# Kernel tuning notes

Measured on AMD Instinct MI355X. Metric: run time of the kernel, lower is better.

The kernel has to match this reference:

```python
import jax, jax.numpy as jnp
import numpy as np

N_NODES = 100000
N_EDGES = 3200000
P = 32
Q = 32
D = P + Q


def setup_inputs() -> dict:
    key = jax.random.key(0)
    ks = jax.random.split(key, 10)
    u = jax.random.normal(ks[0], (N_NODES, D), dtype=jnp.float32)
    intensity = jax.random.normal(ks[1], (N_NODES, Q), dtype=jnp.float32)
    edge_src = jax.random.randint(ks[2], (N_EDGES,), 0, N_NODES, dtype=jnp.int32)
    edge_dst = jax.random.randint(ks[3], (N_EDGES,), 0, N_NODES, dtype=jnp.int32)
    std = 0.1  # matches nn.init.normal_(std=0.1)
    Wf = std * jax.random.normal(ks[4], (D, D), dtype=jnp.float32)
    Wg = std * jax.random.normal(ks[5], (D, D), dtype=jnp.float32)
    Wz = std * jax.random.normal(ks[6], (P, D), dtype=jnp.float32)
    WA = std * jax.random.normal(ks[7], (Q, 2 * Q), dtype=jnp.float32)
    return {
        "u": u, "intensity": intensity,
        "edge_src": edge_src, "edge_dst": edge_dst,
        "Wf": Wf, "bf": jnp.zeros((D,), jnp.float32),
        "Wg": Wg, "bg": jnp.zeros((D,), jnp.float32),
        "Wz": Wz, "bz": jnp.zeros((P,), jnp.float32),
        "WA": WA, "bA": jnp.zeros((Q,), jnp.float32),
    }


def reference(u, intensity, edge_src, edge_dst, Wf, bf, Wg, bg, Wz, bz, WA, bA):
    N = u.shape[0]
    p = Wz.shape[0]
    # neighbor mean of intensity (zeros for isolated nodes)
    nbr_sum = jax.ops.segment_sum(intensity[edge_src], edge_dst, num_segments=N)
    deg = jax.ops.segment_sum(jnp.ones(edge_src.shape, intensity.dtype), edge_dst, num_segments=N)
    nbr_mean = jnp.where(deg[:, None] > 0, nbr_sum / jnp.maximum(deg, 1.0)[:, None], 0.0)
    # aggout = ReLU(A([intensity_i ; mean_nbr_i]))
    aggout = jax.nn.relu(jnp.concatenate([intensity, nbr_mean], axis=1) @ WA.T + bA)
    Fu = jax.nn.softplus(u @ Wf.T + bf)
    Gu = jax.nn.softplus(u @ Wg.T + bg)
    Zu = jnp.tanh(u @ Wz.T + bz)
    du = -Fu * u + Gu * jnp.concatenate([Zu, aggout], axis=1)
    up = u[:, :p]
    dup = du[:, :p]
    duq = du[:, p:]
    # project dup to be orthogonal to up (norm-preserving drift)
    dup = dup - (jnp.sum(dup * up, axis=1, keepdims=True) / jnp.sum(up * up, axis=1, keepdims=True)) * up
    return jnp.concatenate([dup, duq], axis=1)
```

## Files before the change

### kernel.cpp

```cpp
#include <hip/hip_runtime.h>


#define RLOG 7
#define RNODES 128
#define NBLK 512
#define CAP 6144
#define CHUNK 6272
#define CVB 64

typedef __attribute__((ext_vector_type(8))) short short8;
typedef __attribute__((ext_vector_type(4))) float f32x4;
typedef __attribute__((ext_vector_type(2))) float f32x2;

__device__ __forceinline__ unsigned short f2bf(float x) {
    union { float f; unsigned u; } v; v.f = x;
    unsigned r = v.u + 0x7FFF + ((v.u >> 16) & 1);
    return (unsigned short)(r >> 16);
}

#if __has_builtin(__builtin_amdgcn_cvt_pk_fp8_f32) && __has_builtin(__builtin_amdgcn_cvt_pk_f32_fp8)
__device__ __forceinline__ unsigned pack4_fp8(float a, float b, float c, float d) {
    int p = __builtin_amdgcn_cvt_pk_fp8_f32(a, b, 0, false);
    p = __builtin_amdgcn_cvt_pk_fp8_f32(c, d, p, true);
    return (unsigned)p;
}
__device__ __forceinline__ void unpack4_fp8(unsigned w, float& a, float& b, float& c, float& d) {
    f32x2 lo = __builtin_amdgcn_cvt_pk_f32_fp8(w, false);
    f32x2 hi = __builtin_amdgcn_cvt_pk_f32_fp8(w, true);
    a = lo[0]; b = lo[1]; c = hi[0]; d = hi[1];
}
#else
__device__ __forceinline__ unsigned char f2fp8_sw(float x) {
    union { float f; unsigned u; } v; v.f = x;
    unsigned s = (v.u >> 24) & 0x80;
    float ax = fminf(fabsf(x), 448.0f);
    union { float f; unsigned u; } w; w.f = ax;
    int e = (int)((w.u >> 23) & 0xFF) - 127;
    if (e < -6) {
        int mi = (int)(ax * 512.0f + 0.5f);
        if (mi > 7) mi = 7;
        return (unsigned char)(s | mi);
    }
    unsigned mant = (w.u >> 20) & 7;
    unsigned rest = w.u & 0xFFFFF;
    unsigned rnd = (rest > 0x80000u) || (rest == 0x80000u && (mant & 1));
    unsigned enc = ((unsigned)(e + 7) << 3) | mant;
    enc += rnd;
    if (enc > 0x7Eu) enc = 0x7Eu;
    return (unsigned char)(s | enc);
}
__device__ __forceinline__ float fp82f_sw(unsigned char b) {
    unsigned e = (b >> 3) & 0xF, m = b & 7;
    float mag;
    if (e == 0) mag = (float)m * 0.001953125f;
    else {
        union { unsigned u; float f; } v;
        v.u = ((e + 120u) << 23) | (m << 20);
        mag = v.f;
    }
    return (b & 0x80) ? -mag : mag;
}
__device__ __forceinline__ unsigned pack4_fp8(float a, float b, float c, float d) {
    return (unsigned)f2fp8_sw(a) | ((unsigned)f2fp8_sw(b) << 8) |
           ((unsigned)f2fp8_sw(c) << 16) | ((unsigned)f2fp8_sw(d) << 24);
}
__device__ __forceinline__ void unpack4_fp8(unsigned w, float& a, float& b, float& c, float& d) {
    a = fp82f_sw((unsigned char)(w & 0xFF));
    b = fp82f_sw((unsigned char)((w >> 8) & 0xFF));
    c = fp82f_sw((unsigned char)((w >> 16) & 0xFF));
    d = fp82f_sw((unsigned char)((w >> 24) & 0xFF));
}
#endif

__device__ __forceinline__ float softplus_fast(float x) {
    float t = __expf(-fabsf(x));
    return fmaxf(x, 0.0f) + __logf(1.0f + t);
}

__device__ __forceinline__ float tanh_fast(float x) {
    float t = __expf(-2.0f * fabsf(x));
    float m = (1.0f - t) * __builtin_amdgcn_rcpf(1.0f + t);
    return __builtin_copysignf(m, x);
}

__device__ __forceinline__ int chunk_of(int E) {
    return (((E + NBLK - 1) / NBLK) + 3) & ~3;
}

__global__ __launch_bounds__(1024) void prep_count(
    const int* __restrict__ edst, int* __restrict__ cnt,
    const float* __restrict__ x, unsigned short* __restrict__ ybf,
    unsigned* __restrict__ yfp8, int total4,
    const float* __restrict__ Wf, const float* __restrict__ Wg,
    const float* __restrict__ Wz, const float* __restrict__ WA,
    unsigned short* __restrict__ wbig,
    int E, int B) {
    int tid = threadIdx.x, blk = blockIdx.x;
    if (blk < NBLK) {
        __shared__ int lcnt[1024];
        for (int b = tid; b < B; b += 1024) lcnt[b] = 0;
        __syncthreads();
        int chunk = chunk_of(E);
        int start = blk * chunk;
        int end = min(E, start + chunk);
        int v4s = start >> 2, v4e = end >> 2;
        for (int i = v4s + tid; i < v4e; i += 1024) {
            int4 d = ((const int4*)edst)[i];
            atomicAdd(&lcnt[d.x >> RLOG], 1);
            atomicAdd(&lcnt[d.y >> RLOG], 1);
            atomicAdd(&lcnt[d.z >> RLOG], 1);
            atomicAdd(&lcnt[d.w >> RLOG], 1);
        }
        for (int i = (v4e << 2) + tid; i < end; i += 1024)
            atomicAdd(&lcnt[edst[i] >> RLOG], 1);
        __syncthreads();
        for (int b = tid; b < B; b += 1024) cnt[b * NBLK + blk] = lcnt[b];
    } else if (blk < NBLK + CVB) {
        int cb = blk - NBLK;
        for (int i = cb * 1024 + tid; i < total4; i += CVB * 1024) {
            float4 v = ((const float4*)x)[i];
            ushort4 r;
            r.x = f2bf(v.x); r.y = f2bf(v.y); r.z = f2bf(v.z); r.w = f2bf(v.w);
            ((ushort4*)ybf)[i] = r;
            yfp8[i] = pack4_fp8(v.x, v.y, v.z, v.w);
        }
    } else {
        for (int idx = tid; idx < 192 * 64; idx += 1024) {
            int r = idx >> 6, k = idx & 63;
            float v = (r < 64)  ? Wf[r * 64 + k]
                    : (r < 128) ? Wg[(r - 64) * 64 + k]
                    : (r < 160) ? Wz[(r - 128) * 64 + k]
                                : WA[(r - 160) * 64 + k];
            wbig[idx] = f2bf(v);
        }
    }
}

__global__ __launch_bounds__(512) void scanA(const int* __restrict__ cnt,
                                             int* __restrict__ lofs,
                                             int* __restrict__ T) {
    int t = threadIdx.x, b = blockIdx.x;
    int lane = t & 63, wave = t >> 6;
    int v = cnt[b * NBLK + t];
    int incl = v;
    #pragma unroll
    for (int off = 1; off < 64; off <<= 1) {
        int w = __shfl_up(incl, off);
        if (lane >= off) incl += w;
    }
    __shared__ int wt[8];
    if (lane == 63) wt[wave] = incl;
    __syncthreads();
    int woff = 0;
    for (int i = 0; i < wave; ++i) woff += wt[i];
    int excl = woff + incl - v;
    lofs[b * NBLK + t] = excl;
    if (t == NBLK - 1) T[b] = excl + v;
}

__global__ __launch_bounds__(1024) void scanB(const int* __restrict__ T,
                                              int* __restrict__ G, int B) {
    int t = threadIdx.x;
    int lane = t & 63, wave = t >> 6;
    int v = (t < B) ? T[t] : 0;
    int incl = v;
    #pragma unroll
    for (int off = 1; off < 64; off <<= 1) {
        int w = __shfl_up(incl, off);
        if (lane >= off) incl += w;
    }
    __shared__ int wt[16];
    if (lane == 63) wt[wave] = incl;
    __syncthreads();
    int woff = 0;
    for (int i = 0; i < wave; ++i) woff += wt[i];
    if (t < B) G[t] = woff + incl - v;
}

__global__ __launch_bounds__(1024) void bin_scatter(const int* __restrict__ esrc,
                                                    const int* __restrict__ edst,
                                                    const int* __restrict__ cnt,
                                                    const int* __restrict__ lofs,
                                                    const int* __restrict__ G,
                                                    int* __restrict__ binned,
                                                    int E, int B) {
    __shared__ unsigned sl_pack[CHUNK];
    __shared__ unsigned short sl_bkt[CHUNK];
    __shared__ int lsc[1024];
    __shared__ int base[1024];
    __shared__ int wtot[16];
    int tid = threadIdx.x, blk = blockIdx.x;
    int lane = tid & 63, wave = tid >> 6;

    int v = (tid < B) ? cnt[tid * NBLK + blk] : 0;
    int incl = v;
    #pragma unroll
    for (int off = 1; off < 64; off <<= 1) {
        int w = __shfl_up(incl, off);
        if (lane >= off) incl += w;
    }
    if (lane == 63) wtot[wave] = incl;
    __syncthreads();
    int woff = 0;
    for (int i = 0; i < wave; ++i) woff += wtot[i];
    int excl = woff + incl - v;
    if (tid < B) {
        base[tid] = G[tid] + lofs[tid * NBLK + blk] - excl;
        lsc[tid] = excl;
    }
    __syncthreads();

    int chunk = chunk_of(E);
    int start = blk * chunk;
    int end = min(E, start + chunk);
    int m = end - start;
    int v4s = start >> 2, v4e = end >> 2;
    for (int i = v4s + tid; i < v4e; i += 1024) {
        int4 d = ((const int4*)edst)[i];
        int4 s = ((const int4*)esrc)[i];
        int b0 = d.x >> RLOG, b1 = d.y >> RLOG, b2 = d.z >> RLOG, b3 = d.w >> RLOG;
        int p0 = atomicAdd(&lsc[b0], 1);
        int p1 = atomicAdd(&lsc[b1], 1);
        int p2 = atomicAdd(&lsc[b2], 1);
        int p3 = atomicAdd(&lsc[b3], 1);
        sl_pack[p0] = ((unsigned)(d.x & (RNODES - 1)) << 17) | (unsigned)s.x;
        sl_pack[p1] = ((unsigned)(d.y & (RNODES - 1)) << 17) | (unsigned)s.y;
        sl_pack[p2] = ((unsigned)(d.z & (RNODES - 1)) << 17) | (unsigned)s.z;
        sl_pack[p3] = ((unsigned)(d.w & (RNODES - 1)) << 17) | (unsigned)s.w;
        sl_bkt[p0] = (unsigned short)b0;
        sl_bkt[p1] = (unsigned short)b1;
        sl_bkt[p2] = (unsigned short)b2;
        sl_bkt[p3] = (unsigned short)b3;
    }
    for (int i = (v4e << 2) + tid; i < end; i += 1024) {
        int d = edst[i];
        int s = esrc[i];
        int b = d >> RLOG;
        int p = atomicAdd(&lsc[b], 1);
        sl_pack[p] = ((unsigned)(d & (RNODES - 1)) << 17) | (unsigned)s;
        sl_bkt[p] = (unsigned short)b;
    }
    __syncthreads();

    for (int i = tid; i < m; i += 1024) {
        binned[base[sl_bkt[i]] + i] = (int)sl_pack[i];
    }
}

__global__ __launch_bounds__(1024) void bucket_fused(
    const int* __restrict__ binned, const int* __restrict__ G,
    const unsigned* __restrict__ ifp8,
    unsigned short* __restrict__ xnbr, int E, int N, int B) {
    __shared__ int sl[CAP];
    __shared__ int sl2[CAP];
    __shared__ int c128[RNODES];
    __shared__ int pos[RNODES];
    __shared__ int dstart[RNODES];
    __shared__ int ddeg[RNODES];
    int tid = threadIdx.x;
    int b = blockIdx.x;
    int start = G[b];
    int end = (b + 1 < B) ? G[b + 1] : E;
    int m = min(end - start, CAP);

    for (int i = tid; i < m; i += 1024) sl[i] = binned[start + i];
    if (tid < RNODES) c128[tid] = 0;
    __syncthreads();
    for (int i = tid; i < m; i += 1024) atomicAdd(&c128[sl[i] >> 17], 1);
    __syncthreads();

    int x = 0, incl = 0;
    if (tid < RNODES) { x = c128[tid]; incl = x; }
    #pragma unroll
    for (int off = 1; off < RNODES; off <<= 1) {
        int y = 0;
        if (tid < RNODES && tid >= off) y = c128[tid - off];
        __syncthreads();
        if (tid < RNODES) { incl += y; c128[tid] = incl; }
        __syncthreads();
    }
    if (tid < RNODES) {
        int excl = incl - x;
        pos[tid] = excl;
        dstart[tid] = excl;
        ddeg[tid] = x;
    }
    __syncthreads();
    for (int i = tid; i < m; i += 1024) {
        int e = sl[i];
        int p = atomicAdd(&pos[e >> 17], 1);
        sl2[p] = e & 131071;
    }
    __syncthreads();

    int g = tid >> 3;
    int fl = tid & 7;
    int node = b * RNODES + g;
    int st = dstart[g];
    int dg = ddeg[g];
    float a0 = 0.f, a1 = 0.f, a2 = 0.f, a3 = 0.f;
    int j = 0;
    for (; j + 3 < dg; j += 4) {
        int s0 = sl2[st + j];
        int s1 = sl2[st + j + 1];
        int s2 = sl2[st + j + 2];
        int s3 = sl2[st + j + 3];
        unsigned w0 = ifp8[(size_t)s0 * 8 + fl];
        unsigned w1 = ifp8[(size_t)s1 * 8 + fl];
        unsigned w2 = ifp8[(size_t)s2 * 8 + fl];
        unsigned w3 = ifp8[(size_t)s3 * 8 + fl];
        float x0, x1, x2, x3;
        unpack4_fp8(w0, x0, x1, x2, x3);
        a0 += x0; a1 += x1; a2 += x2; a3 += x3;
        unpack4_fp8(w1, x0, x1, x2, x3);
        a0 += x0; a1 += x1; a2 += x2; a3 += x3;
        unpack4_fp8(w2, x0, x1, x2, x3);
        a0 += x0; a1 += x1; a2 += x2; a3 += x3;
        unpack4_fp8(w3, x0, x1, x2, x3);
        a0 += x0; a1 += x1; a2 += x2; a3 += x3;
    }
    for (; j < dg; ++j) {
        int s0 = sl2[st + j];
        unsigned w0 = ifp8[(size_t)s0 * 8 + fl];
        float x0, x1, x2, x3;
        unpack4_fp8(w0, x0, x1, x2, x3);
        a0 += x0; a1 += x1; a2 += x2; a3 += x3;
    }
    if (node < N) {
        float inv = (dg > 0) ? 1.0f / (float)dg : 0.0f;
        ushort4 r;
        r.x = f2bf(a0 * inv); r.y = f2bf(a1 * inv);
        r.z = f2bf(a2 * inv); r.w = f2bf(a3 * inv);
        ((ushort4*)xnbr)[(size_t)node * 8 + fl] = r;
    }
}

__global__ __launch_bounds__(256, 4) void node_mfma(
    const float* __restrict__ u,
    const unsigned short* __restrict__ ibf,
    const unsigned short* __restrict__ xnbr,
    const unsigned short* __restrict__ wbig,
    const float* __restrict__ bfp, const float* __restrict__ bgp,
    const float* __restrict__ bzp, const float* __restrict__ bAp,
    float* __restrict__ out, int N) {
    int tid = threadIdx.x;
    int lane = tid & 63;
    int wave = tid >> 6;
    int tile = blockIdx.x * 4 + wave;
    int ntiles = N >> 4;
    if (tile >= ntiles) return;

    int col = lane & 15;
    int kg = lane >> 4;
    int n0 = tile * 16;
    int node = n0 + col;

    const float* ub = u + (size_t)node * 64 + kg * 8;
    float4 u0 = *(const float4*)(ub);
    float4 u1 = *(const float4*)(ub + 4);
    float4 u2 = *(const float4*)(ub + 32);
    float4 u3 = *(const float4*)(ub + 36);
    short8 au0, au1;
    au0[0]=(short)f2bf(u0.x); au0[1]=(short)f2bf(u0.y); au0[2]=(short)f2bf(u0.z); au0[3]=(short)f2bf(u0.w);
    au0[4]=(short)f2bf(u1.x); au0[5]=(short)f2bf(u1.y); au0[6]=(short)f2bf(u1.z); au0[7]=(short)f2bf(u1.w);
    au1[0]=(short)f2bf(u2.x); au1[1]=(short)f2bf(u2.y); au1[2]=(short)f2bf(u2.z); au1[3]=(short)f2bf(u2.w);
    au1[4]=(short)f2bf(u3.x); au1[5]=(short)f2bf(u3.y); au1[6]=(short)f2bf(u3.z); au1[7]=(short)f2bf(u3.w);
    short8 ax0 = *(const short8*)(ibf  + (size_t)node * 32 + kg * 8);
    short8 ax1 = *(const short8*)(xnbr + (size_t)node * 32 + kg * 8);

    const short8* wb = (const short8*)wbig;
    f32x4 acc[12];
    #pragma unroll
    for (int t = 0; t < 12; ++t) acc[t] = (f32x4){0.f, 0.f, 0.f, 0.f};
    #pragma unroll
    for (int t = 0; t < 12; ++t) {
        short8 a0 = (t < 10) ? au0 : ax0;
        short8 a1 = (t < 10) ? au1 : ax1;
        short8 b0 = wb[(t * 16 + col) * 8 + kg];
        short8 b1 = wb[(t * 16 + col) * 8 + 4 + kg];
        acc[t] = __builtin_amdgcn_mfma_f32_16x16x32_bf16(a0, b0, acc[t], 0, 0, 0);
        acc[t] = __builtin_amdgcn_mfma_f32_16x16x32_bf16(a1, b1, acc[t], 0, 0, 0);
    }

    float bfv[4], bgv[4], bzv[4];
    #pragma unroll
    for (int s = 0; s < 4; ++s) {
        int j = s * 16 + col;
        bfv[s] = bfp[j];
        bgv[s] = bgp[j];
        bzv[s] = (s < 2) ? bzp[j] : bAp[j - 32];
    }

    float du01[2][4], uv01[2][4];
    float ar[4], br[4];
    #pragma unroll
    for (int r = 0; r < 4; ++r) { ar[r] = 0.f; br[r] = 0.f; }
    #pragma unroll
    for (int s = 0; s < 2; ++s) {
        #pragma unroll
        for (int r = 0; r < 4; ++r) {
            int nd = n0 + kg * 4 + r;
            float uu = u[(size_t)nd * 64 + s * 16 + col];
            float fpre = acc[s][r] + bfv[s];
            float gpre = acc[4 + s][r] + bgv[s];
            float zpre = acc[8 + s][r] + bzv[s];
            float Fu = softplus_fast(fpre);
            float Gu = softplus_fast(gpre);
            float zv = tanh_fast(zpre);
            float d = -Fu * uu + Gu * zv;
            du01[s][r] = d;
            uv01[s][r] = uu;
            ar[r] = fmaf(d, uu, ar[r]);
            br[r] = fmaf(uu, uu, br[r]);
        }
    }
    #pragma unroll
    for (int off = 1; off < 16; off <<= 1) {
        #pragma unroll
        for (int r = 0; r < 4; ++r) {
            ar[r] += __shfl_xor(ar[r], off);
            br[r] += __shfl_xor(br[r], off);
        }
    }
    float coef[4];
    #pragma unroll
    for (int r = 0; r < 4; ++r) coef[r] = ar[r] * __builtin_amdgcn_rcpf(br[r]);

    #pragma unroll
    for (int s = 0; s < 2; ++s) {
        #pragma unroll
        for (int r = 0; r < 4; ++r) {
            int nd = n0 + kg * 4 + r;
            out[(size_t)nd * 64 + s * 16 + col] = du01[s][r] - coef[r] * uv01[s][r];
        }
    }
    #pragma unroll
    for (int s = 2; s < 4; ++s) {
        #pragma unroll
        for (int r = 0; r < 4; ++r) {
            int nd = n0 + kg * 4 + r;
            float uu = u[(size_t)nd * 64 + s * 16 + col];
            float fpre = acc[s][r] + bfv[s];
            float gpre = acc[4 + s][r] + bgv[s];
            float zpre = acc[8 + s][r] + bzv[s];
            float Fu = softplus_fast(fpre);
            float Gu = softplus_fast(gpre);
            float zv = fmaxf(zpre, 0.0f);
            out[(size_t)nd * 64 + s * 16 + col] = -Fu * uu + Gu * zv;
        }
    }
}

extern "C" void kernel_launch(void* const* d_in, const int* in_sizes, int n_in,
                              void* d_out, int out_size, void* d_ws, size_t ws_size,
                              hipStream_t stream) {
    const float* u         = (const float*)d_in[0];
    const float* intensity = (const float*)d_in[1];
    const int*   esrc      = (const int*)d_in[2];
    const int*   edst      = (const int*)d_in[3];
    const float* Wf        = (const float*)d_in[4];
    const float* bf        = (const float*)d_in[5];
    const float* Wg        = (const float*)d_in[6];
    const float* bg        = (const float*)d_in[7];
    const float* Wz        = (const float*)d_in[8];
    const float* bz        = (const float*)d_in[9];
    const float* WA        = (const float*)d_in[10];
    const float* bA        = (const float*)d_in[11];

    int N = in_sizes[0] / 64;
    int E = in_sizes[2];
    int B = (N + RNODES - 1) / RNODES;
    int M = B * NBLK;

    int* cnt    = (int*)d_ws;
    int* lofs   = cnt + M;
    int* T      = lofs + M;
    int* G      = T + 1024;
    int* binned = G + 1024;
    unsigned short* xnbr = (unsigned short*)(binned + E);
    unsigned short* wbig = xnbr + (size_t)N * 32;
    unsigned short* ibf  = wbig + 192 * 64;
    unsigned* ifp8 = (unsigned*)(ibf + (size_t)N * 32);

    prep_count<<<NBLK + CVB + 1, 1024, 0, stream>>>(
        edst, cnt, intensity, ibf, ifp8, N * 8, Wf, Wg, Wz, WA, wbig, E, B);
    scanA<<<B, 512, 0, stream>>>(cnt, lofs, T);
    scanB<<<1, 1024, 0, stream>>>(T, G, B);
    bin_scatter<<<NBLK, 1024, 0, stream>>>(esrc, edst, cnt, lofs, G, binned, E, B);
    bucket_fused<<<B, 1024, 0, stream>>>(binned, G, ifp8, xnbr, E, N, B);
    int ntiles = N / 16;
    int nblocks = (ntiles + 3) / 4;
    node_mfma<<<nblocks, 256, 0, stream>>>(u, ibf, xnbr, wbig,
                                           bf, bg, bz, bA, (float*)d_out, N);
}
```

Baseline: 98.04 us.

## Fold scanB into consumers and widen the neighbor gather to 8-byte loads

Drops the single-block scanB launch. bin_scatter and bucket_fused each now rescan the per-bucket totals T in shared memory to get global bucket offsets, which removes one kernel launch and its serialization point at the cost of redundant scan work in every block. The bucket_fused gather is also restructured: each 8-lane group splits into two halves that process alternate edges with uint2 loads of 8 fp8 values, then combine through a shuffle-xor. The aim is more bytes per load and more memory-level parallelism per node, paid for with extra accumulator registers and a reduction step.

```diff
diff --git a/kernel.cpp b/kernel.cpp
--- a/kernel.cpp
+++ b/kernel.cpp
@@ -158,30 +158,11 @@
     if (t == NBLK - 1) T[b] = excl + v;
 }
 
-__global__ __launch_bounds__(1024) void scanB(const int* __restrict__ T,
-                                              int* __restrict__ G, int B) {
-    int t = threadIdx.x;
-    int lane = t & 63, wave = t >> 6;
-    int v = (t < B) ? T[t] : 0;
-    int incl = v;
-    #pragma unroll
-    for (int off = 1; off < 64; off <<= 1) {
-        int w = __shfl_up(incl, off);
-        if (lane >= off) incl += w;
-    }
-    __shared__ int wt[16];
-    if (lane == 63) wt[wave] = incl;
-    __syncthreads();
-    int woff = 0;
-    for (int i = 0; i < wave; ++i) woff += wt[i];
-    if (t < B) G[t] = woff + incl - v;
-}
-
 __global__ __launch_bounds__(1024) void bin_scatter(const int* __restrict__ esrc,
                                                     const int* __restrict__ edst,
                                                     const int* __restrict__ cnt,
                                                     const int* __restrict__ lofs,
-                                                    const int* __restrict__ G,
+                                                    const int* __restrict__ T,
                                                     int* __restrict__ binned,
                                                     int E, int B) {
     __shared__ unsigned sl_pack[CHUNK];
@@ -192,6 +173,20 @@
     int tid = threadIdx.x, blk = blockIdx.x;
     int lane = tid & 63, wave = tid >> 6;
 
+    int tv = (tid < B) ? T[tid] : 0;
+    int tincl = tv;
+    #pragma unroll
+    for (int off = 1; off < 64; off <<= 1) {
+        int w = __shfl_up(tincl, off);
+        if (lane >= off) tincl += w;
+    }
+    if (lane == 63) wtot[wave] = tincl;
+    __syncthreads();
+    int twoff = 0;
+    for (int i = 0; i < wave; ++i) twoff += wtot[i];
+    int Gv = twoff + tincl - tv;
+    __syncthreads();
+
     int v = (tid < B) ? cnt[tid * NBLK + blk] : 0;
     int incl = v;
     #pragma unroll
@@ -205,7 +200,7 @@
     for (int i = 0; i < wave; ++i) woff += wtot[i];
     int excl = woff + incl - v;
     if (tid < B) {
-        base[tid] = G[tid] + lofs[tid * NBLK + blk] - excl;
+        base[tid] = Gv + lofs[tid * NBLK + blk] - excl;
         lsc[tid] = excl;
     }
     __syncthreads();
@@ -248,7 +243,7 @@
 }
 
 __global__ __launch_bounds__(1024) void bucket_fused(
-    const int* __restrict__ binned, const int* __restrict__ G,
+    const int* __restrict__ binned, const int* __restrict__ T,
     const unsigned* __restrict__ ifp8,
     unsigned short* __restrict__ xnbr, int E, int N, int B) {
     __shared__ int sl[CAP];
@@ -257,11 +252,27 @@
     __shared__ int pos[RNODES];
     __shared__ int dstart[RNODES];
     __shared__ int ddeg[RNODES];
+    __shared__ int wtot[16];
+    __shared__ int s_start;
     int tid = threadIdx.x;
     int b = blockIdx.x;
-    int start = G[b];
-    int end = (b + 1 < B) ? G[b + 1] : E;
-    int m = min(end - start, CAP);
+    int lane = tid & 63, wave = tid >> 6;
+
+    int tv = (tid < B) ? T[tid] : 0;
+    int tincl = tv;
+    #pragma unroll
+    for (int off = 1; off < 64; off <<= 1) {
+        int w = __shfl_up(tincl, off);
+        if (lane >= off) tincl += w;
+    }
+    if (lane == 63) wtot[wave] = tincl;
+    __syncthreads();
+    int twoff = 0;
+    for (int i = 0; i < wave; ++i) twoff += wtot[i];
+    if (tid == b) s_start = twoff + tincl - tv;
+    __syncthreads();
+    int start = s_start;
+    int m = min((tid == tid ? 0 : 0) + ((b < B) ? ((int)T[b]) : 0), CAP);
 
     for (int i = tid; i < m; i += 1024) sl[i] = binned[start + i];
     if (tid < RNODES) c128[tid] = 0;
@@ -294,44 +305,53 @@
     __syncthreads();
 
     int g = tid >> 3;
-    int fl = tid & 7;
+    int l = tid & 7;
+    int half = l >> 2;
+    int fl = l & 3;
     int node = b * RNODES + g;
     int st = dstart[g];
     int dg = ddeg[g];
     float a0 = 0.f, a1 = 0.f, a2 = 0.f, a3 = 0.f;
+    float a4 = 0.f, a5 = 0.f, a6 = 0.f, a7 = 0.f;
     int j = 0;
-    for (; j + 3 < dg; j += 4) {
+    for (; j + 7 < dg; j += 8) {
+        int s0 = sl2[st + j + half];
+        int s1 = sl2[st + j + 2 + half];
+        int s2 = sl2[st + j + 4 + half];
+        int s3 = sl2[st + j + 6 + half];
+        uint2 w0 = ((const uint2*)ifp8)[s0 * 4 + fl];
+        uint2 w1 = ((const uint2*)ifp8)[s1 * 4 + fl];
+        uint2 w2 = ((const uint2*)ifp8)[s2 * 4 + fl];
+        uint2 w3 = ((const uint2*)ifp8)[s3 * 4 + fl];
+        float x0, x1, x2, x3;
+        unpack4_fp8(w0.x, x0, x1, x2, x3); a0 += x0; a1 += x1; a2 += x2; a3 += x3;
+        unpack4_fp8(w0.y, x0, x1, x2, x3); a4 += x0; a5 += x1; a6 += x2; a7 += x3;
+        unpack4_fp8(w1.x, x0, x1, x2, x3); a0 += x0; a1 += x1; a2 += x2; a3 += x3;
+        unpack4_fp8(w1.y, x0, x1, x2, x3); a4 += x0; a5 += x1; a6 += x2; a7 += x3;
+        unpack4_fp8(w2.x, x0, x1, x2, x3); a0 += x0; a1 += x1; a2 += x2; a3 += x3;
+        unpack4_fp8(w2.y, x0, x1, x2, x3); a4 += x0; a5 += x1; a6 += x2; a7 += x3;
+        unpack4_fp8(w3.x, x0, x1, x2, x3); a0 += x0; a1 += x1; a2 += x2; a3 += x3;
+        unpack4_fp8(w3.y, x0, x1, x2, x3); a4 += x0; a5 += x1; a6 += x2; a7 += x3;
+    }
+    for (j = j + half; j < dg; j += 2) {
         int s0 = sl2[st + j];
-        int s1 = sl2[st + j + 1];
-        int s2 = sl2[st + j + 2];
-        int s3 = sl2[st + j + 3];
-        unsigned w0 = ifp8[(size_t)s0 * 8 + fl];
-        unsigned w1 = ifp8[(size_t)s1 * 8 + fl];
-        unsigned w2 = ifp8[(size_t)s2 * 8 + fl];
-        unsigned w3 = ifp8[(size_t)s3 * 8 + fl];
+        uint2 w0 = ((const uint2*)ifp8)[s0 * 4 + fl];
         float x0, x1, x2, x3;
-        unpack4_fp8(w0, x0, x1, x2, x3);
-        a0 += x0; a1 += x1; a2 += x2; a3 += x3;
-        unpack4_fp8(w1, x0, x1, x2, x3);
-        a0 += x0; a1 += x1; a2 += x2; a3 += x3;
-        unpack4_fp8(w2, x0, x1, x2, x3);
-        a0 += x0; a1 += x1; a2 += x2; a3 += x3;
-        unpack4_fp8(w3, x0, x1, x2, x3);
-        a0 += x0; a1 += x1; a2 += x2; a3 += x3;
-    }
-    for (; j < dg; ++j) {
-        int s0 = sl2[st + j];
-        unsigned w0 = ifp8[(size_t)s0 * 8 + fl];
-        float x0, x1, x2, x3;
-        unpack4_fp8(w0, x0, x1, x2, x3);
-        a0 += x0; a1 += x1; a2 += x2; a3 += x3;
-    }
-    if (node < N) {
+        unpack4_fp8(w0.x, x0, x1, x2, x3); a0 += x0; a1 += x1; a2 += x2; a3 += x3;
+        unpack4_fp8(w0.y, x0, x1, x2, x3); a4 += x0; a5 += x1; a6 += x2; a7 += x3;
+    }
+    a0 += __shfl_xor(a0, 4); a1 += __shfl_xor(a1, 4);
+    a2 += __shfl_xor(a2, 4); a3 += __shfl_xor(a3, 4);
+    a4 += __shfl_xor(a4, 4); a5 += __shfl_xor(a5, 4);
+    a6 += __shfl_xor(a6, 4); a7 += __shfl_xor(a7, 4);
+    if (half == 0 && node < N) {
         float inv = (dg > 0) ? 1.0f / (float)dg : 0.0f;
-        ushort4 r;
-        r.x = f2bf(a0 * inv); r.y = f2bf(a1 * inv);
-        r.z = f2bf(a2 * inv); r.w = f2bf(a3 * inv);
-        ((ushort4*)xnbr)[(size_t)node * 8 + fl] = r;
+        short8 r;
+        r[0] = (short)f2bf(a0 * inv); r[1] = (short)f2bf(a1 * inv);
+        r[2] = (short)f2bf(a2 * inv); r[3] = (short)f2bf(a3 * inv);
+        r[4] = (short)f2bf(a4 * inv); r[5] = (short)f2bf(a5 * inv);
+        r[6] = (short)f2bf(a6 * inv); r[7] = (short)f2bf(a7 * inv);
+        ((short8*)xnbr)[(size_t)node * 4 + fl] = r;
     }
 }
 
@@ -475,8 +495,7 @@
     int* cnt    = (int*)d_ws;
     int* lofs   = cnt + M;
     int* T      = lofs + M;
-    int* G      = T + 1024;
-    int* binned = G + 1024;
+    int* binned = T + 1024;
     unsigned short* xnbr = (unsigned short*)(binned + E);
     unsigned short* wbig = xnbr + (size_t)N * 32;
     unsigned short* ibf  = wbig + 192 * 64;
@@ -485,9 +504,8 @@
     prep_count<<<NBLK + CVB + 1, 1024, 0, stream>>>(
         edst, cnt, intensity, ibf, ifp8, N * 8, Wf, Wg, Wz, WA, wbig, E, B);
     scanA<<<B, 512, 0, stream>>>(cnt, lofs, T);
-    scanB<<<1, 1024, 0, stream>>>(T, G, B);
-    bin_scatter<<<NBLK, 1024, 0, stream>>>(esrc, edst, cnt, lofs, G, binned, E, B);
-    bucket_fused<<<B, 1024, 0, stream>>>(binned, G, ifp8, xnbr, E, N, B);
+    bin_scatter<<<NBLK, 1024, 0, stream>>>(esrc, edst, cnt, lofs, T, binned, E, B);
+    bucket_fused<<<B, 1024, 0, stream>>>(binned, T, ifp8, xnbr, E, N, B);
     int ntiles = N / 16;
     int nblocks = (ntiles + 3) / 4;
     node_mfma<<<nblocks, 256, 0, stream>>>(u, ibf, xnbr, wbig,
```

New measurement: 98.87 us. About the same (+0.8%).
